# Performance work log

Hardware: AMD Instinct MI355X
Metric: run time of the kernel (lower is better)

Reference implementation:

```python
import jax, jax.numpy as jnp
import numpy as np

L, B, S, E, H, V = 2, 64, 64, 1024, 1024, 32000


def _uni(key, shape, k):
    return jax.random.uniform(key, shape, jnp.float32, -k, k)


def setup_inputs() -> dict:
    key = jax.random.key(0)
    ks = jax.random.split(key, 16)
    k = 1.0 / np.sqrt(H)
    inp = {
        "inputs": jax.random.randint(ks[0], (S, B), 0, V),
        "hidden": jnp.zeros((L, B, H), jnp.float32),
        "emb": jax.random.uniform(ks[1], (V, E), jnp.float32, -0.1, 0.1),
        # per-layer GRU weights stacked on leading L axis (layer0 input = emb = H)
        "Wx": _uni(ks[2], (L, H, H), k),   # linear_W (no bias), used for r gate
        "Ur": _uni(ks[3], (L, H, H), k),
        "br": _uni(ks[4], (L, H), k),
        "Wz": _uni(ks[5], (L, H, H), k),
        "Uz": _uni(ks[6], (L, H, H), k),
        "bz": _uni(ks[7], (L, H), k),
        "Wh": _uni(ks[8], (L, H, H), k),
        "Uh": _uni(ks[9], (L, H, H), k),
        "bh": _uni(ks[10], (L, H), k),
        "dec_W": jax.random.uniform(ks[11], (V, H), jnp.float32, -0.1, 0.1),
        "dec_b": jnp.zeros((V,), jnp.float32),
    }
    return inp


def _gru_cell(x, h, Wx, Ur, br, Wz, Uz, bz, Wh, Uh, bh):
    # faithful to GRU_Hidden.forward (r gate uses linear_W, bias-free W projections)
    r = jax.nn.sigmoid(x @ Wx.T + h @ Ur.T + br)
    z = jax.nn.sigmoid(x @ Wz.T + h @ Uz.T + bz)
    h_cand = jnp.tanh(x @ Wh.T + (r * h) @ Uh.T + bh)
    return (1.0 - z) * h + z * h_cand


def reference(inputs, hidden, emb, Wx, Ur, br, Wz, Uz, bz, Wh, Uh, bh, dec_W, dec_b):
    x_embs = emb[inputs]  # [S, B, E]; dropout is identity (dp_keep_prob = 1.0)
    n_layers = Wx.shape[0]

    def step(h, x_t):
        new_h = []
        inp = x_t
        for l in range(n_layers):
            hl = _gru_cell(inp, h[l], Wx[l], Ur[l], br[l], Wz[l], Uz[l], bz[l], Wh[l], Uh[l], bh[l])
            new_h.append(hl)
            inp = hl
        logits_t = inp @ dec_W.T + dec_b  # [B, V]
        return jnp.stack(new_h), logits_t

    h_final, logits = jax.lax.scan(step, hidden, x_embs)
    return logits, h_final
```

## Files before the change

### kernel.cpp

```cpp
#include <hip/hip_runtime.h>

#define NB_REC 128
#define SBV    131072000

typedef __bf16 bf16x8 __attribute__((ext_vector_type(8)));
typedef float  f32x4  __attribute__((ext_vector_type(4)));
typedef unsigned short u16;

__device__ __forceinline__ u16 f2bf(float f) {
  union { float f; unsigned u; } c; c.f = f;
  return (u16)((c.u + 0x7fffu + ((c.u >> 16) & 1u)) >> 16);
}
__device__ __forceinline__ float sigm(float x) { return 1.f / (1.f + __expf(-x)); }
__device__ __forceinline__ float tanh_f(float x) { return 2.f / (1.f + __expf(-2.f * x)) - 1.f; }


__global__ void k_cvtv(const float* __restrict__ src, u16* __restrict__ dst, int n4) {
  const float4* s4 = (const float4*)src;
  ushort4* d4 = (ushort4*)dst;
  for (int i = blockIdx.x * blockDim.x + threadIdx.x; i < n4; i += gridDim.x * blockDim.x) {
    float4 v = s4[i];
    ushort4 o; o.x = f2bf(v.x); o.y = f2bf(v.y); o.z = f2bf(v.z); o.w = f2bf(v.w);
    d4[i] = o;
  }
}

__global__ void k_pack3(const float* __restrict__ sx, const float* __restrict__ sz,
                        const float* __restrict__ sh, int srcOff, u16* __restrict__ dst) {
  int i = blockIdx.x * blockDim.x + threadIdx.x;
  if (i >= 786432) return;
  int g = i >> 18;
  int r4 = i & 262143;
  const float* s = (g == 0 ? sx : (g == 1 ? sz : sh)) + srcOff;
  float4 v = ((const float4*)s)[r4];
  ushort4 o; o.x = f2bf(v.x); o.y = f2bf(v.y); o.z = f2bf(v.z); o.w = f2bf(v.w);
  ((ushort4*)dst)[i] = o;
}

__global__ void k_embed(const int* __restrict__ idx, const float* __restrict__ emb,
                        u16* __restrict__ xe) {
  int i = blockIdx.x * blockDim.x + threadIdx.x;
  if (i >= 1048576) return;
  int row = i >> 8, k4 = i & 255;
  int e = idx[row];
  float4 v = ((const float4*)emb)[(size_t)e * 256 + k4];
  ushort4 o; o.x = f2bf(v.x); o.y = f2bf(v.y); o.z = f2bf(v.z); o.w = f2bf(v.w);
  ((ushort4*)xe)[i] = o;
}

template<bool BIAS>
__global__ __launch_bounds__(256) void gemm_bt(const u16* __restrict__ A, const u16* __restrict__ Bm,
                                               float* __restrict__ C, const float* __restrict__ bias,
                                               int M, int N, int K, int mtiles) {
  __shared__ u16 As[128 * 32];
  __shared__ u16 Bs[128 * 32];
  const int tid = threadIdx.x;
  const int bm = blockIdx.x % mtiles, bn = blockIdx.x / mtiles;
  const int m0 = bm * 128, n0 = bn * 128;
  const int lane = tid & 63, w = tid >> 6, wm = w & 1, wn = w >> 1;
  const int la = lane & 15, lk = lane >> 4;
  const int srow = tid >> 2, sk = (tid & 3) * 8;
  f32x4 acc[4][4] = {};
  for (int kt = 0; kt < K; kt += 32) {
    const u16* srcA0 = A + (size_t)(m0 + srow) * K + kt + sk;
    const u16* srcA1 = A + (size_t)(m0 + srow + 64) * K + kt + sk;
    const u16* srcB0 = Bm + (size_t)(n0 + srow) * K + kt + sk;
    const u16* srcB1 = Bm + (size_t)(n0 + srow + 64) * K + kt + sk;
    __builtin_amdgcn_global_load_lds((const __attribute__((address_space(1))) void*)srcA0,
        (__attribute__((address_space(3))) void*)((char*)As + tid * 16), 16, 0, 0);
    __builtin_amdgcn_global_load_lds((const __attribute__((address_space(1))) void*)srcA1,
        (__attribute__((address_space(3))) void*)((char*)As + 4096 + tid * 16), 16, 0, 0);
    __builtin_amdgcn_global_load_lds((const __attribute__((address_space(1))) void*)srcB0,
        (__attribute__((address_space(3))) void*)((char*)Bs + tid * 16), 16, 0, 0);
    __builtin_amdgcn_global_load_lds((const __attribute__((address_space(1))) void*)srcB1,
        (__attribute__((address_space(3))) void*)((char*)Bs + 4096 + tid * 16), 16, 0, 0);
    __syncthreads();
    bf16x8 av[4], bv[4];
    #pragma unroll
    for (int m = 0; m < 4; ++m)
      av[m] = *(const bf16x8*)(As + (wm * 64 + m * 16 + la) * 32 + lk * 8);
    #pragma unroll
    for (int n = 0; n < 4; ++n)
      bv[n] = *(const bf16x8*)(Bs + (wn * 64 + n * 16 + la) * 32 + lk * 8);
    #pragma unroll
    for (int m = 0; m < 4; ++m)
      #pragma unroll
      for (int n = 0; n < 4; ++n)
        acc[m][n] = __builtin_amdgcn_mfma_f32_16x16x32_bf16(av[m], bv[n], acc[m][n], 0, 0, 0);
    __syncthreads();
  }
  #pragma unroll
  for (int n = 0; n < 4; ++n) {
    const int gc = n0 + wn * 64 + n * 16 + la;
    const float bb = BIAS ? bias[gc] : 0.f;
    #pragma unroll
    for (int m = 0; m < 4; ++m) {
      const int gr0 = m0 + wm * 64 + m * 16 + lk * 4;
      #pragma unroll
      for (int r = 0; r < 4; ++r)
        C[(size_t)(gr0 + r) * N + gc] = acc[m][n][r] + bb;
    }
  }
}


__device__ __forceinline__ void gbarF(unsigned* flags, unsigned* release, unsigned ph,
                                      int tid, int bid) {
  __syncthreads();
  asm volatile("s_waitcnt vmcnt(0)" ::: "memory");
  if (tid == 0)
    __hip_atomic_store(&flags[bid], ph, __ATOMIC_RELAXED, __HIP_MEMORY_SCOPE_AGENT);
  if (bid == 0) {
    if (tid < 32) {
      const uint4* fp = ((const uint4*)flags) + tid;
      unsigned g = 0;
      while (true) {
        uint4 v;
        asm volatile("global_load_dwordx4 %0, %1, off sc1\ns_waitcnt vmcnt(0)"
                     : "=v"(v) : "v"(fp) : "memory");
        if (v.x >= ph && v.y >= ph && v.z >= ph && v.w >= ph) break;
        __builtin_amdgcn_s_sleep(1);
        if (++g > 50000000u) break;
      }
    }
    __syncthreads();
    if (tid == 0)
      __hip_atomic_store(release, ph, __ATOMIC_RELAXED, __HIP_MEMORY_SCOPE_AGENT);
  } else {
    if (tid == 0) {
      unsigned g = 0;
      while (__hip_atomic_load(release, __ATOMIC_RELAXED, __HIP_MEMORY_SCOPE_AGENT) < ph) {
        __builtin_amdgcn_s_sleep(1);
        if (++g > 50000000u) break;
      }
    }
    __syncthreads();
  }
}

__device__ __forceinline__ void stageF1(const u16* __restrict__ g, char* s, int tid) {
  uint4 t[16];
  #pragma unroll
  for (int i = 0; i < 16; ++i) {
    int c = i * 256 + tid;
    const u16* p = g + (c >> 7) * 1024 + (c & 127) * 8;
    asm volatile("global_load_dwordx4 %0, %1, off sc1" : "=v"(t[i]) : "v"(p));
  }
  asm volatile("s_waitcnt vmcnt(0)" ::: "memory");
  #pragma unroll
  for (int i = 0; i < 16; ++i) {
    int c = i * 256 + tid;
    int row = c >> 7, cb = (c & 127) * 16;
    *(uint4*)(s + ((row * 2048 + cb) ^ ((row & 7) << 4))) = t[i];
  }
}
__device__ __forceinline__ bf16x8 ldsF(const char* s, int row, int ks, int lk) {
  return *(const bf16x8*)(s + ((row * 2048 + ks * 64 + lk * 16) ^ ((row & 7) << 4)));
}

__device__ __forceinline__ void stageH1(const u16* __restrict__ g, int half, char* s, int tid) {
  uint4 t[8];
  #pragma unroll
  for (int i = 0; i < 8; ++i) {
    int c = i * 256 + tid;
    const u16* p = g + (c >> 6) * 1024 + half * 512 + (c & 63) * 8;
    asm volatile("global_load_dwordx4 %0, %1, off sc1" : "=v"(t[i]) : "v"(p));
  }
  asm volatile("s_waitcnt vmcnt(0)" ::: "memory");
  #pragma unroll
  for (int i = 0; i < 8; ++i) {
    int c = i * 256 + tid;
    int row = c >> 6, cb = (c & 63) * 16;
    *(uint4*)(s + ((row * 1024 + cb) ^ ((row & 7) << 4))) = t[i];
  }
}
__device__ __forceinline__ void stageH2(const u16* __restrict__ gA, const u16* __restrict__ gB,
                                        int half, char* sA, char* sB, int tid) {
  uint4 ta[8], tb[8];
  #pragma unroll
  for (int i = 0; i < 8; ++i) {
    int c = i * 256 + tid;
    int row = c >> 6, ce = (c & 63) * 8;
    const u16* pa = gA + row * 1024 + half * 512 + ce;
    const u16* pb = gB + row * 1024 + half * 512 + ce;
    asm volatile("global_load_dwordx4 %0, %1, off sc1" : "=v"(ta[i]) : "v"(pa));
    asm volatile("global_load_dwordx4 %0, %1, off sc1" : "=v"(tb[i]) : "v"(pb));
  }
  asm volatile("s_waitcnt vmcnt(0)" ::: "memory");
  #pragma unroll
  for (int i = 0; i < 8; ++i) {
    int c = i * 256 + tid;
    int row = c >> 6, cb = (c & 63) * 16;
    int off = (row * 1024 + cb) ^ ((row & 7) << 4);
    *(uint4*)(sA + off) = ta[i];
    *(uint4*)(sB + off) = tb[i];
  }
}
__device__ __forceinline__ bf16x8 ldsH(const char* s, int row, int ksl, int lk) {
  return *(const bf16x8*)(s + ((row * 1024 + ksl * 64 + lk * 16) ^ ((row & 7) << 4)));
}

template<bool BIG>
__global__ __launch_bounds__(256) void k_recur(
    const u16* __restrict__ hinitb,
    const float* __restrict__ hidden,
    const float* __restrict__ X0,
    const u16* __restrict__ Ucat0, const u16* __restrict__ Ucat1,
    const u16* __restrict__ Wcat1,
    const float* __restrict__ br, const float* __restrict__ bz, const float* __restrict__ bh,
    u16* __restrict__ H0seq, u16* __restrict__ H1seq,
    u16* __restrict__ RH0, u16* __restrict__ RH1,
    float* __restrict__ houtf,
    unsigned* flags, unsigned* release) {
  extern __shared__ char sMem[];
  char* sA = sMem;
  char* sX = sMem + (BIG ? 65536 : 32768);
  const int tid = threadIdx.x, bid = blockIdx.x;
  const int layer = bid >> 6, r6 = bid & 63, bg = r6 >> 5, cc = r6 & 31;
  const int lane = tid & 63, w = tid >> 6, wm = w & 1, wn = w >> 1;
  const int la = lane & 15, lk = lane >> 4;
  const int rowbase = bg * 32;
  const int b0 = rowbase + wm * 16;
  const int rowA = wm * 16 + la;
  const int j0 = cc * 32 + wn * 16;
  const int jl = j0 + la;
  const u16* Ucat = layer ? Ucat1 : Ucat0;
  u16* Hseq = layer ? H1seq : H0seq;
  u16* RHl = layer ? RH1 : RH0;
  const u16* hinit = hinitb + layer * 65536;

  float h_reg[4], z_reg[4];
  #pragma unroll
  for (int r = 0; r < 4; ++r)
    h_reg[r] = hidden[layer * 65536 + (b0 + lk * 4 + r) * 1024 + jl];
  const float bR = br[layer * 1024 + jl], bZ = bz[layer * 1024 + jl], bH = bh[layer * 1024 + jl];

  const u16* BrR = Ucat + ((size_t)(j0 + la)) * 1024 + lk * 8;
  const u16* BrZ = Ucat + ((size_t)(1024 + j0 + la)) * 1024 + lk * 8;
  const u16* BrH = Ucat + ((size_t)(2048 + j0 + la)) * 1024 + lk * 8;
  const u16* WrR = Wcat1 + ((size_t)(j0 + la)) * 1024 + lk * 8;
  const u16* WrZ = Wcat1 + ((size_t)(1024 + j0 + la)) * 1024 + lk * 8;
  const u16* WrH = Wcat1 + ((size_t)(2048 + j0 + la)) * 1024 + lk * 8;

  unsigned ph = 0;
  for (int i = 0; i <= 64; ++i) {
    const int t = layer ? (i - 1) : i;
    const bool act = layer ? (i >= 1) : (i < 64);
    if (act) {
      const u16* hsrc = ((t == 0) ? hinit : (Hseq + (size_t)(t - 1) * 65536)) + rowbase * 1024;
      const u16* xsrc = H0seq + (size_t)t * 65536 + rowbase * 1024;
      f32x4 accR = {0.f, 0.f, 0.f, 0.f}, accZ = {0.f, 0.f, 0.f, 0.f};
      if (BIG) {
        stageF1(hsrc, sA, tid);
        if (layer) stageF1(xsrc, sX, tid);
        __syncthreads();
        if (layer == 0) {
          #pragma unroll 8
          for (int ks = 0; ks < 32; ++ks) {
            bf16x8 a = ldsF(sA, rowA, ks, lk);
            accR = __builtin_amdgcn_mfma_f32_16x16x32_bf16(a, *(const bf16x8*)(BrR + ks * 32), accR, 0, 0, 0);
            accZ = __builtin_amdgcn_mfma_f32_16x16x32_bf16(a, *(const bf16x8*)(BrZ + ks * 32), accZ, 0, 0, 0);
          }
        } else {
          #pragma unroll 4
          for (int ks = 0; ks < 32; ++ks) {
            bf16x8 a = ldsF(sA, rowA, ks, lk);
            bf16x8 x = ldsF(sX, rowA, ks, lk);
            accR = __builtin_amdgcn_mfma_f32_16x16x32_bf16(a, *(const bf16x8*)(BrR + ks * 32), accR, 0, 0, 0);
            accZ = __builtin_amdgcn_mfma_f32_16x16x32_bf16(a, *(const bf16x8*)(BrZ + ks * 32), accZ, 0, 0, 0);
            accR = __builtin_amdgcn_mfma_f32_16x16x32_bf16(x, *(const bf16x8*)(WrR + ks * 32), accR, 0, 0, 0);
            accZ = __builtin_amdgcn_mfma_f32_16x16x32_bf16(x, *(const bf16x8*)(WrZ + ks * 32), accZ, 0, 0, 0);
          }
        }
      } else {
        for (int half = 0; half < 2; ++half) {
          if (layer == 0) {
            stageH1(hsrc, half, sA, tid);
            __syncthreads();
            #pragma unroll 4
            for (int ksl = 0; ksl < 16; ++ksl) {
              const int ks = half * 16 + ksl;
              bf16x8 a = ldsH(sA, rowA, ksl, lk);
              accR = __builtin_amdgcn_mfma_f32_16x16x32_bf16(a, *(const bf16x8*)(BrR + ks * 32), accR, 0, 0, 0);
              accZ = __builtin_amdgcn_mfma_f32_16x16x32_bf16(a, *(const bf16x8*)(BrZ + ks * 32), accZ, 0, 0, 0);
            }
          } else {
            stageH2(hsrc, xsrc, half, sA, sX, tid);
            __syncthreads();
            #pragma unroll 4
            for (int ksl = 0; ksl < 16; ++ksl) {
              const int ks = half * 16 + ksl;
              bf16x8 a = ldsH(sA, rowA, ksl, lk);
              bf16x8 x = ldsH(sX, rowA, ksl, lk);
              accR = __builtin_amdgcn_mfma_f32_16x16x32_bf16(a, *(const bf16x8*)(BrR + ks * 32), accR, 0, 0, 0);
              accZ = __builtin_amdgcn_mfma_f32_16x16x32_bf16(a, *(const bf16x8*)(BrZ + ks * 32), accZ, 0, 0, 0);
              accR = __builtin_amdgcn_mfma_f32_16x16x32_bf16(x, *(const bf16x8*)(WrR + ks * 32), accR, 0, 0, 0);
              accZ = __builtin_amdgcn_mfma_f32_16x16x32_bf16(x, *(const bf16x8*)(WrZ + ks * 32), accZ, 0, 0, 0);
            }
          }
          __syncthreads();
        }
      }
      #pragma unroll
      for (int r = 0; r < 4; ++r) {
        const int row = b0 + lk * 4 + r;
        float pr = accR[r] + bR, pz = accZ[r] + bZ;
        if (layer == 0) {
          const float* xp = X0 + ((size_t)(t * 64 + row)) * 3072 + jl;
          pr += xp[0]; pz += xp[1024];
        }
        float rv = sigm(pr);
        z_reg[r] = sigm(pz);
        unsigned v = f2bf(rv * h_reg[r]);
        u16* p = RHl + (size_t)(t * 64 + row) * 1024 + jl;
        asm volatile("global_store_short %0, %1, off sc1" :: "v"(p), "v"(v));
      }
    }
    gbarF(flags, release, ++ph, tid, bid);
    if (act) {
      const u16* rhsrc = RHl + (size_t)t * 65536 + rowbase * 1024;
      const u16* xsrc = H0seq + (size_t)t * 65536 + rowbase * 1024;
      f32x4 accH = {0.f, 0.f, 0.f, 0.f};
      if (BIG) {
        stageF1(rhsrc, sA, tid);
        __syncthreads();
        if (layer == 0) {
          #pragma unroll 8
          for (int ks = 0; ks < 32; ++ks) {
            bf16x8 a = ldsF(sA, rowA, ks, lk);
            accH = __builtin_amdgcn_mfma_f32_16x16x32_bf16(a, *(const bf16x8*)(BrH + ks * 32), accH, 0, 0, 0);
          }
        } else {
          #pragma unroll 8
          for (int ks = 0; ks < 32; ++ks) {
            bf16x8 a = ldsF(sA, rowA, ks, lk);
            bf16x8 x = ldsF(sX, rowA, ks, lk);
            accH = __builtin_amdgcn_mfma_f32_16x16x32_bf16(a, *(const bf16x8*)(BrH + ks * 32), accH, 0, 0, 0);
            accH = __builtin_amdgcn_mfma_f32_16x16x32_bf16(x, *(const bf16x8*)(WrH + ks * 32), accH, 0, 0, 0);
          }
        }
      } else {
        for (int half = 0; half < 2; ++half) {
          if (layer == 0) {
            stageH1(rhsrc, half, sA, tid);
            __syncthreads();
            #pragma unroll 4
            for (int ksl = 0; ksl < 16; ++ksl) {
              const int ks = half * 16 + ksl;
              bf16x8 a = ldsH(sA, rowA, ksl, lk);
              accH = __builtin_amdgcn_mfma_f32_16x16x32_bf16(a, *(const bf16x8*)(BrH + ks * 32), accH, 0, 0, 0);
            }
          } else {
            stageH2(rhsrc, xsrc, half, sA, sX, tid);
            __syncthreads();
            #pragma unroll 4
            for (int ksl = 0; ksl < 16; ++ksl) {
              const int ks = half * 16 + ksl;
              bf16x8 a = ldsH(sA, rowA, ksl, lk);
              bf16x8 x = ldsH(sX, rowA, ksl, lk);
              accH = __builtin_amdgcn_mfma_f32_16x16x32_bf16(a, *(const bf16x8*)(BrH + ks * 32), accH, 0, 0, 0);
              accH = __builtin_amdgcn_mfma_f32_16x16x32_bf16(x, *(const bf16x8*)(WrH + ks * 32), accH, 0, 0, 0);
            }
          }
          __syncthreads();
        }
      }
      #pragma unroll
      for (int r = 0; r < 4; ++r) {
        const int row = b0 + lk * 4 + r;
        float pre = accH[r] + bH;
        if (layer == 0) pre += X0[((size_t)(t * 64 + row)) * 3072 + 2048 + jl];
        float hc = tanh_f(pre);
        float hn = h_reg[r] + z_reg[r] * (hc - h_reg[r]);
        h_reg[r] = hn;
        unsigned v = f2bf(hn);
        u16* p = Hseq + (size_t)(t * 64 + row) * 1024 + jl;
        asm volatile("global_store_short %0, %1, off sc1" :: "v"(p), "v"(v));
        if (t == 63) houtf[layer * 65536 + row * 1024 + jl] = hn;
      }
    }
    gbarF(flags, release, ++ph, tid, bid);
  }
}

extern "C" void kernel_launch(void* const* d_in, const int* in_sizes, int n_in,
                              void* d_out, int out_size, void* d_ws, size_t ws_size,
                              hipStream_t stream) {
  const int* inputs = (const int*)d_in[0];
  const float* hidden = (const float*)d_in[1];
  const float* emb = (const float*)d_in[2];
  const float* Wx = (const float*)d_in[3];
  const float* Ur = (const float*)d_in[4];
  const float* br = (const float*)d_in[5];
  const float* Wz = (const float*)d_in[6];
  const float* Uz = (const float*)d_in[7];
  const float* bz = (const float*)d_in[8];
  const float* Wh = (const float*)d_in[9];
  const float* Uh = (const float*)d_in[10];
  const float* bh = (const float*)d_in[11];
  const float* decW = (const float*)d_in[12];
  const float* decb = (const float*)d_in[13];
  float* out = (float*)d_out;

  char* ws = (char*)d_ws;
  size_t off = 0;
  auto alloc = [&](size_t bytes) { char* p = ws + off; off += (bytes + 255) & ~(size_t)255; return p; };
  unsigned* flags = (unsigned*)alloc(4096);
  unsigned* release = flags + 256;
  u16* hinitb = (u16*)alloc((size_t)2 * 64 * 1024 * 2);
  u16* xe     = (u16*)alloc((size_t)4096 * 1024 * 2);
  u16* Wcat0b = (u16*)alloc((size_t)3072 * 1024 * 2);
  u16* Wcat1b = (u16*)alloc((size_t)3072 * 1024 * 2);
  u16* Ucat0b = (u16*)alloc((size_t)3072 * 1024 * 2);
  u16* Ucat1b = (u16*)alloc((size_t)3072 * 1024 * 2);
  u16* decWb  = (u16*)alloc((size_t)32000 * 1024 * 2);
  float* X0   = (float*)alloc((size_t)4096 * 3072 * 4);
  u16* H0seq  = (u16*)alloc((size_t)4096 * 1024 * 2);
  u16* H1seq  = (u16*)alloc((size_t)4096 * 1024 * 2);
  u16* RH0    = (u16*)alloc((size_t)4096 * 1024 * 2);
  u16* RH1    = (u16*)alloc((size_t)4096 * 1024 * 2);

  hipMemsetAsync(flags, 0, 4096, stream);
  k_cvtv<<<128, 256, 0, stream>>>(hidden, hinitb, 32768);
  k_pack3<<<3072, 256, 0, stream>>>(Wx, Wz, Wh, 0, Wcat0b);
  k_pack3<<<3072, 256, 0, stream>>>(Wx, Wz, Wh, 1048576, Wcat1b);
  k_pack3<<<3072, 256, 0, stream>>>(Ur, Uz, Uh, 0, Ucat0b);
  k_pack3<<<3072, 256, 0, stream>>>(Ur, Uz, Uh, 1048576, Ucat1b);
  k_embed<<<4096, 256, 0, stream>>>(inputs, emb, xe);
  k_cvtv<<<4096, 256, 0, stream>>>(decW, decWb, 8192000);

  gemm_bt<false><<<768, 256, 0, stream>>>(xe, Wcat0b, X0, nullptr, 4096, 3072, 1024, 32);

  hipError_t eattr = hipFuncSetAttribute(reinterpret_cast<const void*>(&k_recur<true>),
                                         hipFuncAttributeMaxDynamicSharedMemorySize, 131072);
  if (eattr == hipSuccess) {
    k_recur<true><<<NB_REC, 256, 131072, stream>>>(hinitb, hidden, X0, Ucat0b, Ucat1b, Wcat1b,
                                                   br, bz, bh, H0seq, H1seq, RH0, RH1,
                                                   out + (size_t)SBV, flags, release);
  } else {
    (void)hipFuncSetAttribute(reinterpret_cast<const void*>(&k_recur<false>),
                              hipFuncAttributeMaxDynamicSharedMemorySize, 65536);
    k_recur<false><<<NB_REC, 256, 65536, stream>>>(hinitb, hidden, X0, Ucat0b, Ucat1b, Wcat1b,
                                                   br, bz, bh, H0seq, H1seq, RH0, RH1,
                                                   out + (size_t)SBV, flags, release);
  }

  gemm_bt<true><<<8000, 256, 0, stream>>>(H1seq, decWb, out, decb, 4096, 32000, 1024, 32);
}
```

Baseline: 2.581 ms.

## Replace global grid barrier with per-group dataflow flags in GRU recurrence

The centralized grid barrier (block 0 gathers all flags, then broadcasts a release) is replaced by per-(layer,batch-group) flag arrays. Each block publishes its phase, and consumers poll only the 32 producer flags they depend on. Layer 1 now waits only on layer 0's same-batch-group output for step t, not on every block. This drops the layer-skewed outer loop, so the layers pipeline through point-to-point dependencies, and a stageF2 helper issues the h and x loads together. The cost is more polling traffic spread across blocks, plus a shorter spin timeout that could silently break the dependency under contention.

```diff
diff --git a/kernel.cpp b/kernel.cpp
--- a/kernel.cpp
+++ b/kernel.cpp
@@ -104,38 +104,46 @@
 }
 
 
-__device__ __forceinline__ void gbarF(unsigned* flags, unsigned* release, unsigned ph,
-                                      int tid, int bid) {
+__device__ __forceinline__ void waitg(const unsigned* f, unsigned tgt, int lane) {
+  if (tgt == 0) return;
+  unsigned g = 0;
+  while (true) {
+    bool ok = true;
+    if (lane < 8) {
+      uint4 v; const uint4* p = (const uint4*)f + lane;
+      asm volatile("global_load_dwordx4 %0, %1, off sc1\ns_waitcnt vmcnt(0)"
+                   : "=v"(v) : "v"(p) : "memory");
+      ok = v.x >= tgt && v.y >= tgt && v.z >= tgt && v.w >= tgt;
+    }
+    if (__all(ok)) break;
+    __builtin_amdgcn_s_sleep(1);
+    if (++g > 2000000u) break;
+  }
+}
+
+__device__ __forceinline__ void waitg2(const unsigned* f0, unsigned t0,
+                                       const unsigned* f1, unsigned t1, int lane) {
+  unsigned g = 0;
+  while (true) {
+    bool ok = true;
+    if (lane < 16) {
+      const unsigned* f = (lane < 8) ? f0 : f1;
+      unsigned tgt = (lane < 8) ? t0 : t1;
+      uint4 v; const uint4* p = (const uint4*)f + (lane & 7);
+      asm volatile("global_load_dwordx4 %0, %1, off sc1\ns_waitcnt vmcnt(0)"
+                   : "=v"(v) : "v"(p) : "memory");
+      ok = v.x >= tgt && v.y >= tgt && v.z >= tgt && v.w >= tgt;
+    }
+    if (__all(ok)) break;
+    __builtin_amdgcn_s_sleep(1);
+    if (++g > 2000000u) break;
+  }
+}
+
+__device__ __forceinline__ void arrive(unsigned* myFlag, unsigned val, int tid) {
   __syncthreads();
-  asm volatile("s_waitcnt vmcnt(0)" ::: "memory");
   if (tid == 0)
-    __hip_atomic_store(&flags[bid], ph, __ATOMIC_RELAXED, __HIP_MEMORY_SCOPE_AGENT);
-  if (bid == 0) {
-    if (tid < 32) {
-      const uint4* fp = ((const uint4*)flags) + tid;
-      unsigned g = 0;
-      while (true) {
-        uint4 v;
-        asm volatile("global_load_dwordx4 %0, %1, off sc1\ns_waitcnt vmcnt(0)"
-                     : "=v"(v) : "v"(fp) : "memory");
-        if (v.x >= ph && v.y >= ph && v.z >= ph && v.w >= ph) break;
-        __builtin_amdgcn_s_sleep(1);
-        if (++g > 50000000u) break;
-      }
-    }
-    __syncthreads();
-    if (tid == 0)
-      __hip_atomic_store(release, ph, __ATOMIC_RELAXED, __HIP_MEMORY_SCOPE_AGENT);
-  } else {
-    if (tid == 0) {
-      unsigned g = 0;
-      while (__hip_atomic_load(release, __ATOMIC_RELAXED, __HIP_MEMORY_SCOPE_AGENT) < ph) {
-        __builtin_amdgcn_s_sleep(1);
-        if (++g > 50000000u) break;
-      }
-    }
-    __syncthreads();
-  }
+    asm volatile("global_store_dword %0, %1, off sc1" :: "v"(myFlag), "v"(val) : "memory");
 }
 
 __device__ __forceinline__ void stageF1(const u16* __restrict__ g, char* s, int tid) {
@@ -152,6 +160,27 @@
     int c = i * 256 + tid;
     int row = c >> 7, cb = (c & 127) * 16;
     *(uint4*)(s + ((row * 2048 + cb) ^ ((row & 7) << 4))) = t[i];
+  }
+}
+__device__ __forceinline__ void stageF2(const u16* __restrict__ gA, const u16* __restrict__ gB,
+                                        char* sA, char* sB, int tid) {
+  uint4 ta[16], tb[16];
+  #pragma unroll
+  for (int i = 0; i < 16; ++i) {
+    int c = i * 256 + tid;
+    const u16* pa = gA + (c >> 7) * 1024 + (c & 127) * 8;
+    const u16* pb = gB + (c >> 7) * 1024 + (c & 127) * 8;
+    asm volatile("global_load_dwordx4 %0, %1, off sc1" : "=v"(ta[i]) : "v"(pa));
+    asm volatile("global_load_dwordx4 %0, %1, off sc1" : "=v"(tb[i]) : "v"(pb));
+  }
+  asm volatile("s_waitcnt vmcnt(0)" ::: "memory");
+  #pragma unroll
+  for (int i = 0; i < 16; ++i) {
+    int c = i * 256 + tid;
+    int row = c >> 7, cb = (c & 127) * 16;
+    int off = (row * 2048 + cb) ^ ((row & 7) << 4);
+    *(uint4*)(sA + off) = ta[i];
+    *(uint4*)(sB + off) = tb[i];
   }
 }
 __device__ __forceinline__ bf16x8 ldsF(const char* s, int row, int ks, int lk) {
@@ -211,7 +240,7 @@
     u16* __restrict__ H0seq, u16* __restrict__ H1seq,
     u16* __restrict__ RH0, u16* __restrict__ RH1,
     float* __restrict__ houtf,
-    unsigned* flags, unsigned* release) {
+    unsigned* flags) {
   extern __shared__ char sMem[];
   char* sA = sMem;
   char* sX = sMem + (BIG ? 65536 : 32768);
@@ -228,6 +257,9 @@
   u16* Hseq = layer ? H1seq : H0seq;
   u16* RHl = layer ? RH1 : RH0;
   const u16* hinit = hinitb + layer * 65536;
+  unsigned* fSelf = flags + (layer * 2 + bg) * 32;
+  unsigned* fX    = flags + bg * 32;
+  unsigned* myFlag = fSelf + cc;
 
   float h_reg[4], z_reg[4];
   #pragma unroll
@@ -242,144 +274,146 @@
   const u16* WrZ = Wcat1 + ((size_t)(1024 + j0 + la)) * 1024 + lk * 8;
   const u16* WrH = Wcat1 + ((size_t)(2048 + j0 + la)) * 1024 + lk * 8;
 
-  unsigned ph = 0;
-  for (int i = 0; i <= 64; ++i) {
-    const int t = layer ? (i - 1) : i;
-    const bool act = layer ? (i >= 1) : (i < 64);
-    if (act) {
-      const u16* hsrc = ((t == 0) ? hinit : (Hseq + (size_t)(t - 1) * 65536)) + rowbase * 1024;
-      const u16* xsrc = H0seq + (size_t)t * 65536 + rowbase * 1024;
-      f32x4 accR = {0.f, 0.f, 0.f, 0.f}, accZ = {0.f, 0.f, 0.f, 0.f};
+  for (int t = 0; t < 64; ++t) {
+    const u16* hsrc = ((t == 0) ? hinit : (Hseq + (size_t)(t - 1) * 65536)) + rowbase * 1024;
+    const u16* xsrc = H0seq + (size_t)t * 65536 + rowbase * 1024;
+    f32x4 accR = {0.f, 0.f, 0.f, 0.f}, accZ = {0.f, 0.f, 0.f, 0.f};
+    if (layer == 0) {
+      waitg(fSelf, 2 * t, lane);
       if (BIG) {
         stageF1(hsrc, sA, tid);
-        if (layer) stageF1(xsrc, sX, tid);
         __syncthreads();
-        if (layer == 0) {
-          #pragma unroll 8
-          for (int ks = 0; ks < 32; ++ks) {
-            bf16x8 a = ldsF(sA, rowA, ks, lk);
+        #pragma unroll 8
+        for (int ks = 0; ks < 32; ++ks) {
+          bf16x8 a = ldsF(sA, rowA, ks, lk);
+          accR = __builtin_amdgcn_mfma_f32_16x16x32_bf16(a, *(const bf16x8*)(BrR + ks * 32), accR, 0, 0, 0);
+          accZ = __builtin_amdgcn_mfma_f32_16x16x32_bf16(a, *(const bf16x8*)(BrZ + ks * 32), accZ, 0, 0, 0);
+        }
+      } else {
+        for (int half = 0; half < 2; ++half) {
+          stageH1(hsrc, half, sA, tid);
+          __syncthreads();
+          #pragma unroll 4
+          for (int ksl = 0; ksl < 16; ++ksl) {
+            const int ks = half * 16 + ksl;
+            bf16x8 a = ldsH(sA, rowA, ksl, lk);
             accR = __builtin_amdgcn_mfma_f32_16x16x32_bf16(a, *(const bf16x8*)(BrR + ks * 32), accR, 0, 0, 0);
             accZ = __builtin_amdgcn_mfma_f32_16x16x32_bf16(a, *(const bf16x8*)(BrZ + ks * 32), accZ, 0, 0, 0);
           }
-        } else {
+          __syncthreads();
+        }
+      }
+    } else {
+      waitg2(fSelf, 2 * t, fX, 2 * t + 2, lane);
+      if (BIG) {
+        stageF2(hsrc, xsrc, sA, sX, tid);
+        __syncthreads();
+        #pragma unroll 4
+        for (int ks = 0; ks < 32; ++ks) {
+          bf16x8 a = ldsF(sA, rowA, ks, lk);
+          bf16x8 x = ldsF(sX, rowA, ks, lk);
+          accR = __builtin_amdgcn_mfma_f32_16x16x32_bf16(a, *(const bf16x8*)(BrR + ks * 32), accR, 0, 0, 0);
+          accZ = __builtin_amdgcn_mfma_f32_16x16x32_bf16(a, *(const bf16x8*)(BrZ + ks * 32), accZ, 0, 0, 0);
+          accR = __builtin_amdgcn_mfma_f32_16x16x32_bf16(x, *(const bf16x8*)(WrR + ks * 32), accR, 0, 0, 0);
+          accZ = __builtin_amdgcn_mfma_f32_16x16x32_bf16(x, *(const bf16x8*)(WrZ + ks * 32), accZ, 0, 0, 0);
+        }
+      } else {
+        for (int half = 0; half < 2; ++half) {
+          stageH2(hsrc, xsrc, half, sA, sX, tid);
+          __syncthreads();
           #pragma unroll 4
-          for (int ks = 0; ks < 32; ++ks) {
-            bf16x8 a = ldsF(sA, rowA, ks, lk);
-            bf16x8 x = ldsF(sX, rowA, ks, lk);
+          for (int ksl = 0; ksl < 16; ++ksl) {
+            const int ks = half * 16 + ksl;
+            bf16x8 a = ldsH(sA, rowA, ksl, lk);
+            bf16x8 x = ldsH(sX, rowA, ksl, lk);
             accR = __builtin_amdgcn_mfma_f32_16x16x32_bf16(a, *(const bf16x8*)(BrR + ks * 32), accR, 0, 0, 0);
             accZ = __builtin_amdgcn_mfma_f32_16x16x32_bf16(a, *(const bf16x8*)(BrZ + ks * 32), accZ, 0, 0, 0);
             accR = __builtin_amdgcn_mfma_f32_16x16x32_bf16(x, *(const bf16x8*)(WrR + ks * 32), accR, 0, 0, 0);
             accZ = __builtin_amdgcn_mfma_f32_16x16x32_bf16(x, *(const bf16x8*)(WrZ + ks * 32), accZ, 0, 0, 0);
           }
+          __syncthreads();
+        }
+      }
+    }
+    #pragma unroll
+    for (int r = 0; r < 4; ++r) {
+      const int row = b0 + lk * 4 + r;
+      float pr = accR[r] + bR, pz = accZ[r] + bZ;
+      if (layer == 0) {
+        const float* xp = X0 + ((size_t)(t * 64 + row)) * 3072 + jl;
+        pr += xp[0]; pz += xp[1024];
+      }
+      float rv = sigm(pr);
+      z_reg[r] = sigm(pz);
+      unsigned v = f2bf(rv * h_reg[r]);
+      u16* p = RHl + (size_t)(t * 64 + row) * 1024 + jl;
+      asm volatile("global_store_short %0, %1, off sc1" :: "v"(p), "v"(v));
+    }
+    asm volatile("s_waitcnt vmcnt(0)" ::: "memory");
+    arrive(myFlag, 2 * t + 1, tid);
+    const u16* rhsrc = RHl + (size_t)t * 65536 + rowbase * 1024;
+    f32x4 accH = {0.f, 0.f, 0.f, 0.f};
+    waitg(fSelf, 2 * t + 1, lane);
+    if (BIG) {
+      stageF1(rhsrc, sA, tid);
+      __syncthreads();
+      if (layer == 0) {
+        #pragma unroll 8
+        for (int ks = 0; ks < 32; ++ks) {
+          bf16x8 a = ldsF(sA, rowA, ks, lk);
+          accH = __builtin_amdgcn_mfma_f32_16x16x32_bf16(a, *(const bf16x8*)(BrH + ks * 32), accH, 0, 0, 0);
         }
       } else {
-        for (int half = 0; half < 2; ++half) {
-          if (layer == 0) {
-            stageH1(hsrc, half, sA, tid);
-            __syncthreads();
-            #pragma unroll 4
-            for (int ksl = 0; ksl < 16; ++ksl) {
-              const int ks = half * 16 + ksl;
-              bf16x8 a = ldsH(sA, rowA, ksl, lk);
-              accR = __builtin_amdgcn_mfma_f32_16x16x32_bf16(a, *(const bf16x8*)(BrR + ks * 32), accR, 0, 0, 0);
-              accZ = __builtin_amdgcn_mfma_f32_16x16x32_bf16(a, *(const bf16x8*)(BrZ + ks * 32), accZ, 0, 0, 0);
-            }
-          } else {
-            stageH2(hsrc, xsrc, half, sA, sX, tid);
-            __syncthreads();
-            #pragma unroll 4
-            for (int ksl = 0; ksl < 16; ++ksl) {
-              const int ks = half * 16 + ksl;
-              bf16x8 a = ldsH(sA, rowA, ksl, lk);
-              bf16x8 x = ldsH(sX, rowA, ksl, lk);
-              accR = __builtin_amdgcn_mfma_f32_16x16x32_bf16(a, *(const bf16x8*)(BrR + ks * 32), accR, 0, 0, 0);
-              accZ = __builtin_amdgcn_mfma_f32_16x16x32_bf16(a, *(const bf16x8*)(BrZ + ks * 32), accZ, 0, 0, 0);
-              accR = __builtin_amdgcn_mfma_f32_16x16x32_bf16(x, *(const bf16x8*)(WrR + ks * 32), accR, 0, 0, 0);
-              accZ = __builtin_amdgcn_mfma_f32_16x16x32_bf16(x, *(const bf16x8*)(WrZ + ks * 32), accZ, 0, 0, 0);
-            }
-          }
-          __syncthreads();
+        #pragma unroll 8
+        for (int ks = 0; ks < 32; ++ks) {
+          bf16x8 a = ldsF(sA, rowA, ks, lk);
+          bf16x8 x = ldsF(sX, rowA, ks, lk);
+          accH = __builtin_amdgcn_mfma_f32_16x16x32_bf16(a, *(const bf16x8*)(BrH + ks * 32), accH, 0, 0, 0);
+          accH = __builtin_amdgcn_mfma_f32_16x16x32_bf16(x, *(const bf16x8*)(WrH + ks * 32), accH, 0, 0, 0);
         }
       }
-      #pragma unroll
-      for (int r = 0; r < 4; ++r) {
-        const int row = b0 + lk * 4 + r;
-        float pr = accR[r] + bR, pz = accZ[r] + bZ;
+    } else {
+      const u16* xsrc2 = H0seq + (size_t)t * 65536 + rowbase * 1024;
+      for (int half = 0; half < 2; ++half) {
         if (layer == 0) {
-          const float* xp = X0 + ((size_t)(t * 64 + row)) * 3072 + jl;
-          pr += xp[0]; pz += xp[1024];
-        }
-        float rv = sigm(pr);
-        z_reg[r] = sigm(pz);
-        unsigned v = f2bf(rv * h_reg[r]);
-        u16* p = RHl + (size_t)(t * 64 + row) * 1024 + jl;
-        asm volatile("global_store_short %0, %1, off sc1" :: "v"(p), "v"(v));
-      }
-    }
-    gbarF(flags, release, ++ph, tid, bid);
-    if (act) {
-      const u16* rhsrc = RHl + (size_t)t * 65536 + rowbase * 1024;
-      const u16* xsrc = H0seq + (size_t)t * 65536 + rowbase * 1024;
-      f32x4 accH = {0.f, 0.f, 0.f, 0.f};
-      if (BIG) {
-        stageF1(rhsrc, sA, tid);
-        __syncthreads();
-        if (layer == 0) {
-          #pragma unroll 8
-          for (int ks = 0; ks < 32; ++ks) {
-            bf16x8 a = ldsF(sA, rowA, ks, lk);
+          stageH1(rhsrc, half, sA, tid);
+          __syncthreads();
+          #pragma unroll 4
+          for (int ksl = 0; ksl < 16; ++ksl) {
+            const int ks = half * 16 + ksl;
+            bf16x8 a = ldsH(sA, rowA, ksl, lk);
             accH = __builtin_amdgcn_mfma_f32_16x16x32_bf16(a, *(const bf16x8*)(BrH + ks * 32), accH, 0, 0, 0);
           }
         } else {
-          #pragma unroll 8
-          for (int ks = 0; ks < 32; ++ks) {
-            bf16x8 a = ldsF(sA, rowA, ks, lk);
-            bf16x8 x = ldsF(sX, rowA, ks, lk);
+          stageH2(rhsrc, xsrc2, half, sA, sX, tid);
+          __syncthreads();
+          #pragma unroll 4
+          for (int ksl = 0; ksl < 16; ++ksl) {
+            const int ks = half * 16 + ksl;
+            bf16x8 a = ldsH(sA, rowA, ksl, lk);
+            bf16x8 x = ldsH(sX, rowA, ksl, lk);
             accH = __builtin_amdgcn_mfma_f32_16x16x32_bf16(a, *(const bf16x8*)(BrH + ks * 32), accH, 0, 0, 0);
             accH = __builtin_amdgcn_mfma_f32_16x16x32_bf16(x, *(const bf16x8*)(WrH + ks * 32), accH, 0, 0, 0);
           }
         }
-      } else {
-        for (int half = 0; half < 2; ++half) {
-          if (layer == 0) {
-            stageH1(rhsrc, half, sA, tid);
-            __syncthreads();
-            #pragma unroll 4
-            for (int ksl = 0; ksl < 16; ++ksl) {
-              const int ks = half * 16 + ksl;
-              bf16x8 a = ldsH(sA, rowA, ksl, lk);
-              accH = __builtin_amdgcn_mfma_f32_16x16x32_bf16(a, *(const bf16x8*)(BrH + ks * 32), accH, 0, 0, 0);
-            }
-          } else {
-            stageH2(rhsrc, xsrc, half, sA, sX, tid);
-            __syncthreads();
-            #pragma unroll 4
-            for (int ksl = 0; ksl < 16; ++ksl) {
-              const int ks = half * 16 + ksl;
-              bf16x8 a = ldsH(sA, rowA, ksl, lk);
-              bf16x8 x = ldsH(sX, rowA, ksl, lk);
-              accH = __builtin_amdgcn_mfma_f32_16x16x32_bf16(a, *(const bf16x8*)(BrH + ks * 32), accH, 0, 0, 0);
-              accH = __builtin_amdgcn_mfma_f32_16x16x32_bf16(x, *(const bf16x8*)(WrH + ks * 32), accH, 0, 0, 0);
-            }
-          }
-          __syncthreads();
-        }
+        __syncthreads();
       }
-      #pragma unroll
-      for (int r = 0; r < 4; ++r) {
-        const int row = b0 + lk * 4 + r;
-        float pre = accH[r] + bH;
-        if (layer == 0) pre += X0[((size_t)(t * 64 + row)) * 3072 + 2048 + jl];
-        float hc = tanh_f(pre);
-        float hn = h_reg[r] + z_reg[r] * (hc - h_reg[r]);
-        h_reg[r] = hn;
-        unsigned v = f2bf(hn);
-        u16* p = Hseq + (size_t)(t * 64 + row) * 1024 + jl;
-        asm volatile("global_store_short %0, %1, off sc1" :: "v"(p), "v"(v));
-        if (t == 63) houtf[layer * 65536 + row * 1024 + jl] = hn;
-      }
-    }
-    gbarF(flags, release, ++ph, tid, bid);
+    }
+    #pragma unroll
+    for (int r = 0; r < 4; ++r) {
+      const int row = b0 + lk * 4 + r;
+      float pre = accH[r] + bH;
+      if (layer == 0) pre += X0[((size_t)(t * 64 + row)) * 3072 + 2048 + jl];
+      float hc = tanh_f(pre);
+      float hn = h_reg[r] + z_reg[r] * (hc - h_reg[r]);
+      h_reg[r] = hn;
+      unsigned v = f2bf(hn);
+      u16* p = Hseq + (size_t)(t * 64 + row) * 1024 + jl;
+      asm volatile("global_store_short %0, %1, off sc1" :: "v"(p), "v"(v));
+      if (t == 63) houtf[layer * 65536 + row * 1024 + jl] = hn;
+    }
+    asm volatile("s_waitcnt vmcnt(0)" ::: "memory");
+    arrive(myFlag, 2 * t + 2, tid);
   }
 }
 
@@ -406,7 +440,6 @@
   size_t off = 0;
   auto alloc = [&](size_t bytes) { char* p = ws + off; off += (bytes + 255) & ~(size_t)255; return p; };
   unsigned* flags = (unsigned*)alloc(4096);
-  unsigned* release = flags + 256;
   u16* hinitb = (u16*)alloc((size_t)2 * 64 * 1024 * 2);
   u16* xe     = (u16*)alloc((size_t)4096 * 1024 * 2);
   u16* Wcat0b = (u16*)alloc((size_t)3072 * 1024 * 2);
@@ -436,13 +469,13 @@
   if (eattr == hipSuccess) {
     k_recur<true><<<NB_REC, 256, 131072, stream>>>(hinitb, hidden, X0, Ucat0b, Ucat1b, Wcat1b,
                                                    br, bz, bh, H0seq, H1seq, RH0, RH1,
-                                                   out + (size_t)SBV, flags, release);
+                                                   out + (size_t)SBV, flags);
   } else {
     (void)hipFuncSetAttribute(reinterpret_cast<const void*>(&k_recur<false>),
                               hipFuncAttributeMaxDynamicSharedMemorySize, 65536);
     k_recur<false><<<NB_REC, 256, 65536, stream>>>(hinitb, hidden, X0, Ucat0b, Ucat1b, Wcat1b,
                                                    br, bz, bh, H0seq, H1seq, RH0, RH1,
-                                                   out + (size_t)SBV, flags, release);
+                                                   out + (size_t)SBV, flags);
   }
 
   gemm_bt<true><<<8000, 256, 0, stream>>>(H1seq, decWb, out, decb, 4096, 32000, 1024, 32);
```

Result: no change. 2.540 ms (-1.6%).
